# Optimization experiments

Measured on AMD Instinct MI355X. Metric: run time of the kernel, lower is better.

The kernel has to match this reference:

```python
import jax, jax.numpy as jnp
import numpy as np


def setup_inputs() -> dict:
    key = jax.random.key(0)
    ks = jax.random.split(key, 6)
    B, N, D, Dm, Do = 4, 512, 64, 64, 64
    vertices = jax.random.normal(ks[0], (B, N, D), dtype=jnp.float32)
    mask = jax.random.randint(ks[1], (B, N), 0, 2).astype(bool)
    W_msg = jax.random.normal(ks[2], (Dm, 2 * D), dtype=jnp.float32) / np.sqrt(2 * D).astype(np.float32)
    b_msg = jnp.zeros((Dm,), dtype=jnp.float32)
    W_node = jax.random.normal(ks[3], (Do, D + Dm), dtype=jnp.float32) / np.sqrt(D + Dm).astype(np.float32)
    b_node = jnp.zeros((Do,), dtype=jnp.float32)
    return {"vertices": vertices, "mask": mask, "W_msg": W_msg, "b_msg": b_msg,
            "W_node": W_node, "b_node": b_node}


def reference(vertices, mask, W_msg, b_msg, W_node, b_node):
    # vertices: (B,N,D); mask: (B,N) bool
    D = vertices.shape[-1]
    # message_layer(cat(v_i, v_j)) == v_i @ Wi^T + v_j @ Wj^T + b  (split weight)
    Wi, Wj = W_msg[:, :D], W_msg[:, D:]
    a = jnp.einsum('bnd,md->bnm', vertices, Wi)   # (B,N,Dm) src-half
    c = jnp.einsum('bnd,md->bnm', vertices, Wj)   # (B,N,Dm) dst-half
    msg = jax.nn.relu(a[:, :, None, :] + c[:, None, :, :] + b_msg)  # (B,N,N,Dm)
    pair_mask = (mask[:, :, None] & mask[:, None, :])[..., None]    # (B,N,N,1)
    msg = jnp.where(pair_mask, msg, jnp.zeros((), msg.dtype))
    agg = msg.sum(axis=2)                                           # (B,N,Dm)
    h = jnp.concatenate([vertices, agg], axis=-1)                   # (B,N,D+Dm)
    out = jax.nn.relu(jnp.einsum('bnd,od->bno', h, W_node) + b_node)
    return out
```

## Files before the change

kernel.cpp:

```cpp
#include <hip/hip_runtime.h>
#include <hip/hip_bf16.h>


typedef float  f32x4  __attribute__((ext_vector_type(4)));
typedef float  v2f    __attribute__((ext_vector_type(2)));
typedef short  bf16x8 __attribute__((ext_vector_type(8)));
typedef unsigned short u16;

__device__ __forceinline__ v2f pk_add(v2f a, v2f b) {
    v2f d; asm("v_pk_add_f32 %0, %1, %2" : "=v"(d) : "v"(a), "v"(b)); return d;
}
__device__ __forceinline__ u16 bf16_of(float x) {
    __hip_bfloat16 b = __float2bfloat16(x);
    return *(u16*)&b;
}
__device__ __forceinline__ bf16x8 cvt8(const float* p) {
    float4 x = *(const float4*)p, y = *(const float4*)(p + 4);
    float v[8] = {x.x, x.y, x.z, x.w, y.x, y.y, y.z, y.w};
    bf16x8 r;
#pragma unroll
    for (int i = 0; i < 8; ++i) r[i] = (short)bf16_of(v[i]);
    return r;
}
__device__ __forceinline__ void cvt8_hl(const float* p, bf16x8& h, bf16x8& l) {
    float4 x = *(const float4*)p, y = *(const float4*)(p + 4);
    float v[8] = {x.x, x.y, x.z, x.w, y.x, y.y, y.z, y.w};
#pragma unroll
    for (int i = 0; i < 8; ++i) {
        u16 hb = bf16_of(v[i]);
        h[i] = (short)hb;
        unsigned int u = (unsigned)hb << 16;
        l[i] = (short)bf16_of(v[i] - *(float*)&u);
    }
}

__global__ __launch_bounds__(1024) void fused_gb7(
    const float* __restrict__ V, const int* __restrict__ mask,
    const float* __restrict__ Wmsg, const float* __restrict__ bmsg,
    const float* __restrict__ Wn, const float* __restrict__ bn,
    float* __restrict__ out)
{
    __shared__ float buf[9792];
    u16*   vt    = (u16*)buf;
    float* part  = buf;
    float* maskf = buf + 8192;
    float* a_s   = buf + 8704;
    float* agg_s = buf + 9248;

    const int tid  = threadIdx.x;
    const int l    = tid & 63;
    const int w    = tid >> 6;
    const int g    = l >> 4;
    const int l15  = l & 15;
    const int mh   = w >> 3;
    const int jg   = w & 7;
    const int bb   = blockIdx.x >> 6;
    const int i0   = blockIdx.x * 8;
    const int iloc = (blockIdx.x & 63) * 8;
    const float* Vb = V + (size_t)bb * 512 * 64;

    auto stage_half = [&](int h) {
#pragma unroll
        for (int q = 0; q < 4; ++q) {
            int idx = tid + q * 1024;
            int row = idx >> 4;
            int c4  = (idx & 15) << 2;
            float4 v4 = *(const float4*)&Vb[(h * 256 + row) * 64 + c4];
            ushort4 us;
            us.x = bf16_of(v4.x); us.y = bf16_of(v4.y);
            us.z = bf16_of(v4.z); us.w = bf16_of(v4.w);
            int byte = (row << 7) + (((c4 << 1)) ^ ((row & 7) << 4));
            *(ushort4*)((char*)vt + byte) = us;
        }
    };

    stage_half(0);
    if (tid < 512) maskf[tid] = mask[bb * 512 + tid] ? 0.f : -1e30f;

    bf16x8 bWj[2][2];
#pragma unroll
    for (int mtp = 0; mtp < 2; ++mtp) {
        int mrow = (mh * 2 + mtp) * 16 + l15;
#pragma unroll
        for (int kh = 0; kh < 2; ++kh)
            bWj[mtp][kh] = cvt8(Wmsg + mrow * 128 + 64 + (g << 3) + (kh << 5));
    }

    f32x4 acc_o1 = {0.f, 0.f, 0.f, 0.f};
    bf16x8 bWn2[2] = {};
    float bn_m = 0.f;
    if (w < 4) {
        bf16x8 aVh[2], aVl[2], bWih[2], bWil[2], bWn1[2];
#pragma unroll
        for (int kh = 0; kh < 2; ++kh) {
            cvt8_hl(V + (i0 + (l15 & 7)) * 64 + (g << 3) + (kh << 5), aVh[kh], aVl[kh]);
            cvt8_hl(Wmsg + (w * 16 + l15) * 128 + (g << 3) + (kh << 5), bWih[kh], bWil[kh]);
            bWn1[kh] = cvt8(Wn + (w * 16 + l15) * 128 + (g << 3) + (kh << 5));
            bWn2[kh] = cvt8(Wn + (w * 16 + l15) * 128 + 64 + (g << 3) + (kh << 5));
        }
        f32x4 acc_a = {0.f, 0.f, 0.f, 0.f};
#pragma unroll
        for (int kh = 0; kh < 2; ++kh) {
            acc_a = __builtin_amdgcn_mfma_f32_16x16x32_bf16(aVh[kh], bWih[kh], acc_a, 0, 0, 0);
            acc_a = __builtin_amdgcn_mfma_f32_16x16x32_bf16(aVl[kh], bWih[kh], acc_a, 0, 0, 0);
            acc_a = __builtin_amdgcn_mfma_f32_16x16x32_bf16(aVh[kh], bWil[kh], acc_a, 0, 0, 0);
            acc_o1 = __builtin_amdgcn_mfma_f32_16x16x32_bf16(aVh[kh], bWn1[kh], acc_o1, 0, 0, 0);
            acc_o1 = __builtin_amdgcn_mfma_f32_16x16x32_bf16(aVl[kh], bWn1[kh], acc_o1, 0, 0, 0);
        }
        float bm_m = bmsg[w * 16 + l15];
        bn_m = bn[w * 16 + l15];
        if (g < 2) {
#pragma unroll
            for (int i = 0; i < 4; ++i)
                a_s[(g * 4 + i) * 68 + w * 16 + l15] = acc_a[i] + bm_m;
        }
    }
    __syncthreads();

    float nar[2][8];
#pragma unroll
    for (int mtp = 0; mtp < 2; ++mtp) {
        int m = (mh * 2 + mtp) * 16 + l15;
#pragma unroll
        for (int r = 0; r < 8; ++r) nar[mtp][r] = -a_s[r * 68 + m];
    }
    v2f p2[2][8];
#pragma unroll
    for (int mtp = 0; mtp < 2; ++mtp)
#pragma unroll
        for (int r = 0; r < 8; ++r) p2[mtp][r] = (v2f){0.f, 0.f};

    auto compute_half = [&](int h) {
#pragma unroll
        for (int t = 0; t < 2; ++t) {
            int jbase = jg * 32 + t * 16;
            bf16x8 aV[2];
#pragma unroll
            for (int kh = 0; kh < 2; ++kh) {
                int jrow = jbase + l15;
                int byte = (jrow << 7) + ((((g << 4) + (kh << 6))) ^ ((jrow & 7) << 4));
                aV[kh] = *(const bf16x8*)((const char*)vt + byte);
            }
            f32x4 mf = *(const f32x4*)&maskf[h * 256 + jbase + g * 4];
#pragma unroll
            for (int mtp = 0; mtp < 2; ++mtp) {
                f32x4 acc = {0.f, 0.f, 0.f, 0.f};
                acc = __builtin_amdgcn_mfma_f32_16x16x32_bf16(aV[0], bWj[mtp][0], acc, 0, 0, 0);
                acc = __builtin_amdgcn_mfma_f32_16x16x32_bf16(aV[1], bWj[mtp][1], acc, 0, 0, 0);
                float cm0 = acc[0] + mf[0], cm1 = acc[1] + mf[1];
                float cm2 = acc[2] + mf[2], cm3 = acc[3] + mf[3];
#pragma unroll
                for (int r = 0; r < 8; ++r) {
                    float n = nar[mtp][r];
                    v2f mxa = { fmaxf(cm0, n), fmaxf(cm1, n) };
                    v2f mxb = { fmaxf(cm2, n), fmaxf(cm3, n) };
                    p2[mtp][r] = pk_add(p2[mtp][r], mxa);
                    p2[mtp][r] = pk_add(p2[mtp][r], mxb);
                }
            }
        }
    };

    compute_half(0);
    __syncthreads();
    stage_half(1);
    __syncthreads();
    compute_half(1);

    float pr[2][8];
#pragma unroll
    for (int mtp = 0; mtp < 2; ++mtp)
#pragma unroll
        for (int r = 0; r < 8; ++r) {
            float v = p2[mtp][r].x + p2[mtp][r].y;
            v += __shfl_xor(v, 16);
            v += __shfl_xor(v, 32);
            pr[mtp][r] = v;
        }
    __syncthreads();
    if (l < 16) {
#pragma unroll
        for (int mtp = 0; mtp < 2; ++mtp)
#pragma unroll
            for (int r = 0; r < 8; ++r)
                part[jg * 512 + r * 64 + (mh * 2 + mtp) * 16 + l15] = pr[mtp][r];
    }
    __syncthreads();

    if (tid < 512) {
        int r = tid >> 6, m = tid & 63;
        float s = 0.f;
#pragma unroll
        for (int q = 0; q < 8; ++q) s += part[q * 512 + r * 64 + m];
        s = fmaf(512.f, a_s[r * 68 + m], s);
        s = (maskf[iloc + r] == 0.f) ? s : 0.f;
        agg_s[r * 68 + m] = s;
    }
    __syncthreads();

    if (w < 4) {
        bf16x8 aAgg[2];
#pragma unroll
        for (int kh = 0; kh < 2; ++kh)
            aAgg[kh] = cvt8(&agg_s[(l15 & 7) * 68 + (g << 3) + (kh << 5)]);
        f32x4 accO = acc_o1;
        accO = __builtin_amdgcn_mfma_f32_16x16x32_bf16(aAgg[0], bWn2[0], accO, 0, 0, 0);
        accO = __builtin_amdgcn_mfma_f32_16x16x32_bf16(aAgg[1], bWn2[1], accO, 0, 0, 0);
        if (g < 2) {
#pragma unroll
            for (int i = 0; i < 4; ++i)
                out[(i0 + g * 4 + i) * 64 + w * 16 + l15] = fmaxf(accO[i] + bn_m, 0.f);
        }
    }
}

extern "C" void kernel_launch(void* const* d_in, const int* in_sizes, int n_in,
                              void* d_out, int out_size, void* d_ws, size_t ws_size,
                              hipStream_t stream) {
    const float* V    = (const float*)d_in[0];
    const int*   mask = (const int*)d_in[1];
    const float* Wmsg = (const float*)d_in[2];
    const float* bmsg = (const float*)d_in[3];
    const float* Wn   = (const float*)d_in[4];
    const float* bn   = (const float*)d_in[5];
    float* outp = (float*)d_out;

    const int BN = in_sizes[1];
    fused_gb7<<<dim3(BN / 8), dim3(1024), 0, stream>>>(V, mask, Wmsg, bmsg, Wn, bn, outp);
}
```

Before: 18.39 us.

## Compute node projections in fp32 scalar FMAs with weights staged in LDS

Replaces the split-bf16 MFMA computation of the src-half message projection and the node output projection with plain fp32 FMA dot products. Wmsg and the Wn halves are first staged into padded LDS arrays. This removes the hi/lo bf16 conversion work and the extra MFMAs, and it also makes those projections exact fp32. In exchange it adds LDS footprint, an extra up-front weight load and sync, and scalar dot-product loops of length 64 per thread. It also drops one barrier before the partial-sum write.

```diff
diff --git a/kernel.cpp b/kernel.cpp
--- a/kernel.cpp
+++ b/kernel.cpp
@@ -22,30 +22,22 @@
     for (int i = 0; i < 8; ++i) r[i] = (short)bf16_of(v[i]);
     return r;
 }
-__device__ __forceinline__ void cvt8_hl(const float* p, bf16x8& h, bf16x8& l) {
-    float4 x = *(const float4*)p, y = *(const float4*)(p + 4);
-    float v[8] = {x.x, x.y, x.z, x.w, y.x, y.y, y.z, y.w};
-#pragma unroll
-    for (int i = 0; i < 8; ++i) {
-        u16 hb = bf16_of(v[i]);
-        h[i] = (short)hb;
-        unsigned int u = (unsigned)hb << 16;
-        l[i] = (short)bf16_of(v[i] - *(float*)&u);
-    }
-}
-
-__global__ __launch_bounds__(1024) void fused_gb7(
+
+__global__ __launch_bounds__(1024) void fused_gb8(
     const float* __restrict__ V, const int* __restrict__ mask,
     const float* __restrict__ Wmsg, const float* __restrict__ bmsg,
     const float* __restrict__ Wn, const float* __restrict__ bn,
     float* __restrict__ out)
 {
-    __shared__ float buf[9792];
+    __shared__ float buf[14144];
+    float* wm    = buf;
     u16*   vt    = (u16*)buf;
-    float* part  = buf;
-    float* maskf = buf + 8192;
-    float* a_s   = buf + 8704;
-    float* agg_s = buf + 9248;
+    float* wn2   = buf;
+    float* wn1   = buf + 8320;
+    float* part  = buf + 8320;
+    float* maskf = buf + 12544;
+    float* a_s   = buf + 13056;
+    float* agg_s = buf + 13600;
 
     const int tid  = threadIdx.x;
     const int l    = tid & 63;
@@ -59,6 +51,49 @@
     const int iloc = (blockIdx.x & 63) * 8;
     const float* Vb = V + (size_t)bb * 512 * 64;
 
+#pragma unroll
+    for (int k = 0; k < 2; ++k) {
+        int f4 = tid + k * 1024;
+        int mm = f4 >> 5, dd = (f4 & 31) << 2;
+        *(float4*)&wm[mm * 130 + dd] = ((const float4*)Wmsg)[f4];
+    }
+    {
+        int oo = tid >> 4, kk = (tid & 15) << 2;
+        *(float4*)&wn1[oo * 66 + kk] = *(const float4*)&Wn[oo * 128 + kk];
+    }
+    if (tid < 512) maskf[tid] = mask[bb * 512 + tid] ? 0.f : -1e30f;
+    __syncthreads();
+
+    bf16x8 bWj[2][2];
+#pragma unroll
+    for (int mtp = 0; mtp < 2; ++mtp) {
+        int mrow = (mh * 2 + mtp) * 16 + l15;
+#pragma unroll
+        for (int kh = 0; kh < 2; ++kh)
+            bWj[mtp][kh] = cvt8(&wm[mrow * 130 + 64 + (g << 3) + (kh << 5)]);
+    }
+
+    float o1 = 0.f;
+    if (tid < 512) {
+        int m = l;
+        int row = __builtin_amdgcn_readfirstlane(i0 + w);
+        const float* v = V + row * 64;
+        float sa = bmsg[m], so = bn[m];
+#pragma unroll
+        for (int d0 = 0; d0 < 64; d0 += 4) {
+            float4 va = *(const float4*)&v[d0];
+            float4 wa = *(float4*)&wm[m * 130 + d0];
+            float4 wo = *(float4*)&wn1[m * 66 + d0];
+            sa = fmaf(va.x, wa.x, sa); sa = fmaf(va.y, wa.y, sa);
+            sa = fmaf(va.z, wa.z, sa); sa = fmaf(va.w, wa.w, sa);
+            so = fmaf(va.x, wo.x, so); so = fmaf(va.y, wo.y, so);
+            so = fmaf(va.z, wo.z, so); so = fmaf(va.w, wo.w, so);
+        }
+        a_s[w * 68 + m] = sa;
+        o1 = so;
+    }
+    __syncthreads();
+
     auto stage_half = [&](int h) {
 #pragma unroll
         for (int q = 0; q < 4; ++q) {
@@ -69,53 +104,10 @@
             ushort4 us;
             us.x = bf16_of(v4.x); us.y = bf16_of(v4.y);
             us.z = bf16_of(v4.z); us.w = bf16_of(v4.w);
-            int byte = (row << 7) + (((c4 << 1)) ^ ((row & 7) << 4));
+            int byte = (row << 7) + ((c4 << 1) ^ ((row & 7) << 4));
             *(ushort4*)((char*)vt + byte) = us;
         }
     };
-
-    stage_half(0);
-    if (tid < 512) maskf[tid] = mask[bb * 512 + tid] ? 0.f : -1e30f;
-
-    bf16x8 bWj[2][2];
-#pragma unroll
-    for (int mtp = 0; mtp < 2; ++mtp) {
-        int mrow = (mh * 2 + mtp) * 16 + l15;
-#pragma unroll
-        for (int kh = 0; kh < 2; ++kh)
-            bWj[mtp][kh] = cvt8(Wmsg + mrow * 128 + 64 + (g << 3) + (kh << 5));
-    }
-
-    f32x4 acc_o1 = {0.f, 0.f, 0.f, 0.f};
-    bf16x8 bWn2[2] = {};
-    float bn_m = 0.f;
-    if (w < 4) {
-        bf16x8 aVh[2], aVl[2], bWih[2], bWil[2], bWn1[2];
-#pragma unroll
-        for (int kh = 0; kh < 2; ++kh) {
-            cvt8_hl(V + (i0 + (l15 & 7)) * 64 + (g << 3) + (kh << 5), aVh[kh], aVl[kh]);
-            cvt8_hl(Wmsg + (w * 16 + l15) * 128 + (g << 3) + (kh << 5), bWih[kh], bWil[kh]);
-            bWn1[kh] = cvt8(Wn + (w * 16 + l15) * 128 + (g << 3) + (kh << 5));
-            bWn2[kh] = cvt8(Wn + (w * 16 + l15) * 128 + 64 + (g << 3) + (kh << 5));
-        }
-        f32x4 acc_a = {0.f, 0.f, 0.f, 0.f};
-#pragma unroll
-        for (int kh = 0; kh < 2; ++kh) {
-            acc_a = __builtin_amdgcn_mfma_f32_16x16x32_bf16(aVh[kh], bWih[kh], acc_a, 0, 0, 0);
-            acc_a = __builtin_amdgcn_mfma_f32_16x16x32_bf16(aVl[kh], bWih[kh], acc_a, 0, 0, 0);
-            acc_a = __builtin_amdgcn_mfma_f32_16x16x32_bf16(aVh[kh], bWil[kh], acc_a, 0, 0, 0);
-            acc_o1 = __builtin_amdgcn_mfma_f32_16x16x32_bf16(aVh[kh], bWn1[kh], acc_o1, 0, 0, 0);
-            acc_o1 = __builtin_amdgcn_mfma_f32_16x16x32_bf16(aVl[kh], bWn1[kh], acc_o1, 0, 0, 0);
-        }
-        float bm_m = bmsg[w * 16 + l15];
-        bn_m = bn[w * 16 + l15];
-        if (g < 2) {
-#pragma unroll
-            for (int i = 0; i < 4; ++i)
-                a_s[(g * 4 + i) * 68 + w * 16 + l15] = acc_a[i] + bm_m;
-        }
-    }
-    __syncthreads();
 
     float nar[2][8];
 #pragma unroll
@@ -161,6 +153,8 @@
         }
     };
 
+    stage_half(0);
+    __syncthreads();
     compute_half(0);
     __syncthreads();
     stage_half(1);
@@ -177,7 +171,6 @@
             v += __shfl_xor(v, 32);
             pr[mtp][r] = v;
         }
-    __syncthreads();
     if (l < 16) {
 #pragma unroll
         for (int mtp = 0; mtp < 2; ++mtp)
@@ -187,8 +180,12 @@
     }
     __syncthreads();
 
+    {
+        int oo = tid >> 4, kk = (tid & 15) << 2;
+        *(float4*)&wn2[oo * 66 + kk] = *(const float4*)&Wn[oo * 128 + 64 + kk];
+    }
     if (tid < 512) {
-        int r = tid >> 6, m = tid & 63;
+        int r = w, m = l;
         float s = 0.f;
 #pragma unroll
         for (int q = 0; q < 8; ++q) s += part[q * 512 + r * 64 + m];
@@ -198,19 +195,17 @@
     }
     __syncthreads();
 
-    if (w < 4) {
-        bf16x8 aAgg[2];
-#pragma unroll
-        for (int kh = 0; kh < 2; ++kh)
-            aAgg[kh] = cvt8(&agg_s[(l15 & 7) * 68 + (g << 3) + (kh << 5)]);
-        f32x4 accO = acc_o1;
-        accO = __builtin_amdgcn_mfma_f32_16x16x32_bf16(aAgg[0], bWn2[0], accO, 0, 0, 0);
-        accO = __builtin_amdgcn_mfma_f32_16x16x32_bf16(aAgg[1], bWn2[1], accO, 0, 0, 0);
-        if (g < 2) {
-#pragma unroll
-            for (int i = 0; i < 4; ++i)
-                out[(i0 + g * 4 + i) * 64 + w * 16 + l15] = fmaxf(accO[i] + bn_m, 0.f);
-        }
+    if (tid < 512) {
+        int r = w, m = l;
+        float s = o1;
+#pragma unroll
+        for (int k = 0; k < 64; k += 4) {
+            float4 h4 = *(float4*)&agg_s[r * 68 + k];
+            float4 w4 = *(float4*)&wn2[m * 66 + k];
+            s = fmaf(h4.x, w4.x, s); s = fmaf(h4.y, w4.y, s);
+            s = fmaf(h4.z, w4.z, s); s = fmaf(h4.w, w4.w, s);
+        }
+        out[(i0 + r) * 64 + m] = fmaxf(s, 0.f);
     }
 }
 
@@ -226,5 +221,5 @@
     float* outp = (float*)d_out;
 
     const int BN = in_sizes[1];
-    fused_gb7<<<dim3(BN / 8), dim3(1024), 0, stream>>>(V, mask, Wmsg, bmsg, Wn, bn, outp);
-}
+    fused_gb8<<<dim3(BN / 8), dim3(1024), 0, stream>>>(V, mask, Wmsg, bmsg, Wn, bn, outp);
+}
```

Measured after the change: 26.15 us. 1.42x slower.

## Halve rows per block, double grid, and double-buffer vertex staging in LDS

Applied to the files above, without the earlier changes.

Each block now handles 4 query rows with 512 threads instead of 8 rows with 1024 threads, doubling the grid to 512 blocks. Both halves of the bf16 vertex tile get their own LDS buffer, so the second half is staged up front, removing one barrier and the stage/compute serialization. The aim is more blocks to spread across CUs and fewer syncs. In exchange, each block re-stages the full 512-row vertex tile for only 4 rows, doubling global reads and conversion work, and LDS use per block roughly doubles.

```diff
diff --git a/kernel.cpp b/kernel.cpp
--- a/kernel.cpp
+++ b/kernel.cpp
@@ -34,48 +34,49 @@
     }
 }
 
-__global__ __launch_bounds__(1024) void fused_gb7(
+__global__ __launch_bounds__(512, 4) void fused_gb9(
     const float* __restrict__ V, const int* __restrict__ mask,
     const float* __restrict__ Wmsg, const float* __restrict__ bmsg,
     const float* __restrict__ Wn, const float* __restrict__ bn,
     float* __restrict__ out)
 {
-    __shared__ float buf[9792];
-    u16*   vt    = (u16*)buf;
+    __shared__ float buf[17440];
+    u16*   vt0   = (u16*)buf;
+    u16*   vt1   = (u16*)(buf + 8192);
     float* part  = buf;
-    float* maskf = buf + 8192;
-    float* a_s   = buf + 8704;
-    float* agg_s = buf + 9248;
+    float* maskf = buf + 16384;
+    float* a_s   = buf + 16896;
+    float* agg_s = buf + 17168;
 
     const int tid  = threadIdx.x;
     const int l    = tid & 63;
     const int w    = tid >> 6;
     const int g    = l >> 4;
     const int l15  = l & 15;
-    const int mh   = w >> 3;
-    const int jg   = w & 7;
-    const int bb   = blockIdx.x >> 6;
-    const int i0   = blockIdx.x * 8;
-    const int iloc = (blockIdx.x & 63) * 8;
+    const int mh   = w >> 2;
+    const int jgg  = w & 3;
+    const int bb   = blockIdx.x >> 7;
+    const int i0   = blockIdx.x * 4;
+    const int iloc = (blockIdx.x & 127) * 4;
     const float* Vb = V + (size_t)bb * 512 * 64;
 
-    auto stage_half = [&](int h) {
-#pragma unroll
-        for (int q = 0; q < 4; ++q) {
-            int idx = tid + q * 1024;
+    auto stage_half = [&](int h, u16* vt) {
+#pragma unroll
+        for (int q = 0; q < 8; ++q) {
+            int idx = tid + q * 512;
             int row = idx >> 4;
             int c4  = (idx & 15) << 2;
             float4 v4 = *(const float4*)&Vb[(h * 256 + row) * 64 + c4];
             ushort4 us;
             us.x = bf16_of(v4.x); us.y = bf16_of(v4.y);
             us.z = bf16_of(v4.z); us.w = bf16_of(v4.w);
-            int byte = (row << 7) + (((c4 << 1)) ^ ((row & 7) << 4));
+            int byte = (row << 7) + ((c4 << 1) ^ ((row & 7) << 4));
             *(ushort4*)((char*)vt + byte) = us;
         }
     };
 
-    stage_half(0);
-    if (tid < 512) maskf[tid] = mask[bb * 512 + tid] ? 0.f : -1e30f;
+    stage_half(0, vt0);
+    maskf[tid] = mask[bb * 512 + tid] ? 0.f : -1e30f;
 
     bf16x8 bWj[2][2];
 #pragma unroll
@@ -86,14 +87,14 @@
             bWj[mtp][kh] = cvt8(Wmsg + mrow * 128 + 64 + (g << 3) + (kh << 5));
     }
 
-    f32x4 acc_o1 = {0.f, 0.f, 0.f, 0.f};
+    f32x4  acc_o1 = {0.f, 0.f, 0.f, 0.f};
     bf16x8 bWn2[2] = {};
-    float bn_m = 0.f;
+    float  bn_m = 0.f;
     if (w < 4) {
         bf16x8 aVh[2], aVl[2], bWih[2], bWil[2], bWn1[2];
 #pragma unroll
         for (int kh = 0; kh < 2; ++kh) {
-            cvt8_hl(V + (i0 + (l15 & 7)) * 64 + (g << 3) + (kh << 5), aVh[kh], aVl[kh]);
+            cvt8_hl(V + (i0 + (l15 & 3)) * 64 + (g << 3) + (kh << 5), aVh[kh], aVl[kh]);
             cvt8_hl(Wmsg + (w * 16 + l15) * 128 + (g << 3) + (kh << 5), bWih[kh], bWil[kh]);
             bWn1[kh] = cvt8(Wn + (w * 16 + l15) * 128 + (g << 3) + (kh << 5));
             bWn2[kh] = cvt8(Wn + (w * 16 + l15) * 128 + 64 + (g << 3) + (kh << 5));
@@ -101,39 +102,39 @@
         f32x4 acc_a = {0.f, 0.f, 0.f, 0.f};
 #pragma unroll
         for (int kh = 0; kh < 2; ++kh) {
-            acc_a = __builtin_amdgcn_mfma_f32_16x16x32_bf16(aVh[kh], bWih[kh], acc_a, 0, 0, 0);
-            acc_a = __builtin_amdgcn_mfma_f32_16x16x32_bf16(aVl[kh], bWih[kh], acc_a, 0, 0, 0);
-            acc_a = __builtin_amdgcn_mfma_f32_16x16x32_bf16(aVh[kh], bWil[kh], acc_a, 0, 0, 0);
+            acc_a  = __builtin_amdgcn_mfma_f32_16x16x32_bf16(aVh[kh], bWih[kh], acc_a, 0, 0, 0);
+            acc_a  = __builtin_amdgcn_mfma_f32_16x16x32_bf16(aVl[kh], bWih[kh], acc_a, 0, 0, 0);
+            acc_a  = __builtin_amdgcn_mfma_f32_16x16x32_bf16(aVh[kh], bWil[kh], acc_a, 0, 0, 0);
             acc_o1 = __builtin_amdgcn_mfma_f32_16x16x32_bf16(aVh[kh], bWn1[kh], acc_o1, 0, 0, 0);
             acc_o1 = __builtin_amdgcn_mfma_f32_16x16x32_bf16(aVl[kh], bWn1[kh], acc_o1, 0, 0, 0);
         }
         float bm_m = bmsg[w * 16 + l15];
         bn_m = bn[w * 16 + l15];
-        if (g < 2) {
+        if (g == 0) {
 #pragma unroll
             for (int i = 0; i < 4; ++i)
-                a_s[(g * 4 + i) * 68 + w * 16 + l15] = acc_a[i] + bm_m;
-        }
-    }
-    __syncthreads();
-
-    float nar[2][8];
+                a_s[i * 68 + w * 16 + l15] = acc_a[i] + bm_m;
+        }
+    }
+    __syncthreads();
+
+    float nar[2][4];
 #pragma unroll
     for (int mtp = 0; mtp < 2; ++mtp) {
         int m = (mh * 2 + mtp) * 16 + l15;
 #pragma unroll
-        for (int r = 0; r < 8; ++r) nar[mtp][r] = -a_s[r * 68 + m];
-    }
-    v2f p2[2][8];
+        for (int r = 0; r < 4; ++r) nar[mtp][r] = -a_s[r * 68 + m];
+    }
+    v2f p2[2][4];
 #pragma unroll
     for (int mtp = 0; mtp < 2; ++mtp)
 #pragma unroll
-        for (int r = 0; r < 8; ++r) p2[mtp][r] = (v2f){0.f, 0.f};
-
-    auto compute_half = [&](int h) {
-#pragma unroll
-        for (int t = 0; t < 2; ++t) {
-            int jbase = jg * 32 + t * 16;
+        for (int r = 0; r < 4; ++r) p2[mtp][r] = (v2f){0.f, 0.f};
+
+    auto compute_half = [&](int h, const u16* vt) {
+#pragma unroll
+        for (int t = 0; t < 4; ++t) {
+            int jbase = jgg * 64 + t * 16;
             bf16x8 aV[2];
 #pragma unroll
             for (int kh = 0; kh < 2; ++kh) {
@@ -150,7 +151,7 @@
                 float cm0 = acc[0] + mf[0], cm1 = acc[1] + mf[1];
                 float cm2 = acc[2] + mf[2], cm3 = acc[3] + mf[3];
 #pragma unroll
-                for (int r = 0; r < 8; ++r) {
+                for (int r = 0; r < 4; ++r) {
                     float n = nar[mtp][r];
                     v2f mxa = { fmaxf(cm0, n), fmaxf(cm1, n) };
                     v2f mxb = { fmaxf(cm2, n), fmaxf(cm3, n) };
@@ -161,37 +162,34 @@
         }
     };
 
-    compute_half(0);
-    __syncthreads();
-    stage_half(1);
-    __syncthreads();
-    compute_half(1);
-
-    float pr[2][8];
+    stage_half(1, vt1);
+    compute_half(0, vt0);
+    __syncthreads();
+    compute_half(1, vt1);
+
+    float pr[2][4];
 #pragma unroll
     for (int mtp = 0; mtp < 2; ++mtp)
 #pragma unroll
-        for (int r = 0; r < 8; ++r) {
+        for (int r = 0; r < 4; ++r) {
             float v = p2[mtp][r].x + p2[mtp][r].y;
             v += __shfl_xor(v, 16);
             v += __shfl_xor(v, 32);
             pr[mtp][r] = v;
         }
-    __syncthreads();
     if (l < 16) {
 #pragma unroll
         for (int mtp = 0; mtp < 2; ++mtp)
 #pragma unroll
-            for (int r = 0; r < 8; ++r)
-                part[jg * 512 + r * 64 + (mh * 2 + mtp) * 16 + l15] = pr[mtp][r];
-    }
-    __syncthreads();
-
-    if (tid < 512) {
+            for (int r = 0; r < 4; ++r)
+                part[jgg * 256 + r * 64 + (mh * 2 + mtp) * 16 + l15] = pr[mtp][r];
+    }
+    __syncthreads();
+
+    if (tid < 256) {
         int r = tid >> 6, m = tid & 63;
-        float s = 0.f;
-#pragma unroll
-        for (int q = 0; q < 8; ++q) s += part[q * 512 + r * 64 + m];
+        float s = part[r * 64 + m] + part[256 + r * 64 + m]
+                + part[512 + r * 64 + m] + part[768 + r * 64 + m];
         s = fmaf(512.f, a_s[r * 68 + m], s);
         s = (maskf[iloc + r] == 0.f) ? s : 0.f;
         agg_s[r * 68 + m] = s;
@@ -202,14 +200,14 @@
         bf16x8 aAgg[2];
 #pragma unroll
         for (int kh = 0; kh < 2; ++kh)
-            aAgg[kh] = cvt8(&agg_s[(l15 & 7) * 68 + (g << 3) + (kh << 5)]);
+            aAgg[kh] = cvt8(&agg_s[(l15 & 3) * 68 + (g << 3) + (kh << 5)]);
         f32x4 accO = acc_o1;
         accO = __builtin_amdgcn_mfma_f32_16x16x32_bf16(aAgg[0], bWn2[0], accO, 0, 0, 0);
         accO = __builtin_amdgcn_mfma_f32_16x16x32_bf16(aAgg[1], bWn2[1], accO, 0, 0, 0);
-        if (g < 2) {
+        if (g == 0) {
 #pragma unroll
             for (int i = 0; i < 4; ++i)
-                out[(i0 + g * 4 + i) * 64 + w * 16 + l15] = fmaxf(accO[i] + bn_m, 0.f);
+                out[(i0 + i) * 64 + w * 16 + l15] = fmaxf(accO[i] + bn_m, 0.f);
         }
     }
 }
@@ -226,5 +224,5 @@
     float* outp = (float*)d_out;
 
     const int BN = in_sizes[1];
-    fused_gb7<<<dim3(BN / 8), dim3(1024), 0, stream>>>(V, mask, Wmsg, bmsg, Wn, bn, outp);
-}
+    fused_gb9<<<dim3(BN / 4), dim3(512), 0, stream>>>(V, mask, Wmsg, bmsg, Wn, bn, outp);
+}
```

After: 20.15 us. +9.6%, slower.
